# Optimization experiments

Hardware: AMD Instinct MI355X
Metric: run time of the kernel (lower is better)

Reference implementation:

```python
import jax, jax.numpy as jnp
import numpy as np

DIM = 512
NUM_ITEM = 2048
K = 10


def setup_inputs() -> dict:
    key = jax.random.key(0)
    k1, k2, k3 = jax.random.split(key, 3)
    input1 = jax.random.normal(k1, (16, DIM, 32, 32), dtype=jnp.float32)
    input2 = jax.random.normal(k2, (16, DIM, 32, 32), dtype=jnp.float32)
    stdv = 1.0 / np.sqrt(DIM)
    mempool = jax.random.uniform(k3, (NUM_ITEM, DIM), minval=-stdv, maxval=stdv, dtype=jnp.float32)
    return {"input1": input1, "input2": input2, "mempool": mempool}


def _memorize(x, mempool):
    # x: [B, C, H, W] with C == DIM
    B, C, H, W = x.shape
    q = jnp.transpose(x, (0, 2, 3, 1)).reshape(-1, C)      # [N, C]
    att = jax.nn.softmax(q @ mempool.T, axis=1)            # [N, num_item]
    val, idx = jax.lax.top_k(att, K)                       # [N, K]
    val = jax.nn.softmax(val, axis=1)                      # renormalize top-k
    # scatter(val into zeros) @ mempool == gather rows of mempool and combine
    out = jnp.einsum('nk,nkd->nd', val, mempool[idx])      # [N, C]
    return jnp.transpose(out.reshape(B, H, W, C), (0, 3, 1, 2))


def reference(input1, input2, mempool):
    return (_memorize(input1, mempool), _memorize(input2, mempool))
```

## Files before the change

kernel.cpp:

```cpp
#include <hip/hip_runtime.h>
#include <math.h>

typedef __attribute__((ext_vector_type(4))) float f4;
typedef __attribute__((ext_vector_type(8))) short bf16x8;
typedef __attribute__((ext_vector_type(4))) unsigned short u16x4;
typedef unsigned int u32;
typedef unsigned short u16;

#define DIMC  512
#define NITEM 2048
#define TK    10
#define WSP   (NITEM * DIMC)

#define TPB    512
#define PXB    64
#define RIT    256
#define NRND   8
#define NSLICE 16

#define MP_B   0
#define MP_PL  16384
#define SSTR   66
#define Q_B    67584
#define Q_PL   4096
#define LDS_BYTES 79872
#define MV_F 0
#define MI_F 5120
#define MM_F 10240
#define MS_F 10752
#define WB_F 11264
#define IB_F 11904

#define KSWZ(i) (((i) ^ ((i) >> 2)) & 3)

__device__ __forceinline__ u32 bf16_rne(float f) {
    u32 u = __float_as_uint(f);
    return (u + 0x7fffu + ((u >> 16) & 1u)) >> 16;
}

__global__ __launch_bounds__(256)
void preconv_kernel(const float* __restrict__ mp, u16* __restrict__ ws)
{
    int idx = (blockIdx.x * 256 + threadIdx.x) * 4;
    int i  = idx >> 9;
    int k0 = idx & 511;
    f4 v = *(const f4*)(mp + (size_t)i * 512 + k0);
    int s  = k0 >> 5, kl = k0 & 31;
    int pos = s * 32 + ((kl >> 2) & 3) * 8 + (kl >> 4) * 4;
    u16x4 p0, p1, p2;
#pragma unroll
    for (int e = 0; e < 4; ++e) {
        float f  = v[e];
        u32 b0   = bf16_rne(f);  float f0 = __uint_as_float(b0 << 16);
        float r1 = f - f0;
        u32 b1   = bf16_rne(r1); float f1 = __uint_as_float(b1 << 16);
        float r2 = r1 - f1;
        u32 b2   = bf16_rne(r2);
        p0[e] = (u16)b0; p1[e] = (u16)b1; p2[e] = (u16)b2;
    }
    size_t base = (size_t)i * 512 + pos;
    *(u16x4*)(ws + 0 * WSP + base) = p0;
    *(u16x4*)(ws + 1 * WSP + base) = p1;
    *(u16x4*)(ws + 2 * WSP + base) = p2;
}

__global__ __launch_bounds__(TPB, 4)
void memorize_mfma(const float* __restrict__ x0, const float* __restrict__ x1,
                   const float* __restrict__ mp, const u16* __restrict__ ws,
                   float* __restrict__ out)
{
    extern __shared__ char ldsb[];
    float* ldsf = (float*)ldsb;

    const int t    = threadIdx.x;
    const int lane = t & 63;
    const int w    = t >> 6;
    const int blk  = blockIdx.x;
    const int img  = blk >> 4;
    const int n0   = (blk & 15) * PXB;
    const int b    = img & 15;

    const float* x  = (img < 16) ? x0 : x1;
    const float* xb = x + (size_t)b * (DIMC * 1024);
    float* ob = out + (img < 16 ? (size_t)0 : (size_t)16 * DIMC * 1024)
                    + (size_t)b * (DIMC * 1024);

    const int l15 = lane & 15;
    const int lh  = lane >> 4;
    const int ksw = lh ^ KSWZ(l15);

    const int qp = t & 63;
    const int g  = t >> 6;

    float tv[TK]; int tix[TK];
#pragma unroll
    for (int q = 0; q < TK; ++q) { tv[q] = -INFINITY; tix[q] = 0x7fffffff; }
    float rm = -INFINITY, rs = 0.0f;

    const int scl  = t & 31;
    const int spx  = (t >> 5) << 2;
    const int spos = (((scl >> 2) & 3) << 3) + ((scl >> 4) << 2) + (scl & 3);
    const int sslot = spos >> 3;
    const int soff  = (spos & 7) << 1;

    const char* qb = ldsb + Q_B + (l15 << 6) + (ksw << 4);
    const char* ab = ldsb + MP_B + (size_t)((w << 5) + l15) * 64 + (ksw << 4);

    const int itq = lane >> 2;
    const int slo = lane & 3;
    const int ksrc = slo ^ KSWZ(itq);

#pragma unroll 1
    for (int r = 0; r < NRND; ++r) {
        f4 acc[2][4];
#pragma unroll
        for (int mt = 0; mt < 2; ++mt)
#pragma unroll
            for (int nt = 0; nt < 4; ++nt) acc[mt][nt] = (f4){0.f, 0.f, 0.f, 0.f};

#pragma unroll 1
        for (int s = 0; s < NSLICE; ++s) {
            __syncthreads();

            {
#pragma unroll
                for (int p = 0; p < 3; ++p) {
#pragma unroll
                    for (int qg = 0; qg < 2; ++qg) {
                        int I = (w << 5) + (qg << 4);
                        const u16* src = ws + (size_t)p * WSP
                                       + (size_t)(r * RIT + I + itq) * 512
                                       + (s << 5) + (ksrc << 3);
                        char* dst = ldsb + MP_B + p * MP_PL + I * 64;
                        __builtin_amdgcn_global_load_lds(
                            (const __attribute__((address_space(1))) u32*)src,
                            (__attribute__((address_space(3))) u32*)dst, 16, 0, 0);
                    }
                }
            }

            {
                const float* src = xb + (size_t)((s << 5) + scl) * 1024 + n0 + spx;
                f4 v = *(const f4*)src;
#pragma unroll
                for (int e = 0; e < 4; ++e) {
                    int px = spx + e;
                    float f  = v[e];
                    u32 b0   = bf16_rne(f);  float f0 = __uint_as_float(b0 << 16);
                    float r1 = f - f0;
                    u32 b1   = bf16_rne(r1); float f1 = __uint_as_float(b1 << 16);
                    float r2 = r1 - f1;
                    u32 b2   = bf16_rne(r2);
                    int ro = Q_B + (px << 6) + (((sslot ^ KSWZ(px)) << 4) | soff);
                    *(u16*)(ldsb + ro)            = (u16)b0;
                    *(u16*)(ldsb + ro + Q_PL)     = (u16)b1;
                    *(u16*)(ldsb + ro + 2 * Q_PL) = (u16)b2;
                }
            }
            __syncthreads();

            bf16x8 bq[4][3];
#pragma unroll
            for (int nt = 0; nt < 4; ++nt)
#pragma unroll
                for (int p = 0; p < 3; ++p)
                    bq[nt][p] = *(const bf16x8*)(qb + p * Q_PL + nt * 1024);

#pragma unroll
            for (int mt = 0; mt < 2; ++mt) {
                bf16x8 a0 = *(const bf16x8*)(ab + 0 * MP_PL + mt * 1024);
                bf16x8 a1 = *(const bf16x8*)(ab + 1 * MP_PL + mt * 1024);
                bf16x8 a2 = *(const bf16x8*)(ab + 2 * MP_PL + mt * 1024);
#pragma unroll
                for (int nt = 0; nt < 4; ++nt) {
                    f4 c = acc[mt][nt];
                    c = __builtin_amdgcn_mfma_f32_16x16x32_bf16(a0, bq[nt][0], c, 0, 0, 0);
                    c = __builtin_amdgcn_mfma_f32_16x16x32_bf16(a0, bq[nt][1], c, 0, 0, 0);
                    c = __builtin_amdgcn_mfma_f32_16x16x32_bf16(a1, bq[nt][0], c, 0, 0, 0);
                    c = __builtin_amdgcn_mfma_f32_16x16x32_bf16(a0, bq[nt][2], c, 0, 0, 0);
                    c = __builtin_amdgcn_mfma_f32_16x16x32_bf16(a1, bq[nt][1], c, 0, 0, 0);
                    c = __builtin_amdgcn_mfma_f32_16x16x32_bf16(a2, bq[nt][0], c, 0, 0, 0);
                    acc[mt][nt] = c;
                }
            }
        }

        __syncthreads();
#pragma unroll
        for (int mt = 0; mt < 2; ++mt) {
#pragma unroll
            for (int nt = 0; nt < 4; ++nt) {
                int row = (w << 5) + (mt << 4) + (lh << 2);
                int col = (nt << 4) + l15;
                float* sp = ldsf + row * SSTR + col;
                sp[0 * SSTR] = acc[mt][nt][0];
                sp[1 * SSTR] = acc[mt][nt][1];
                sp[2 * SSTR] = acc[mt][nt][2];
                sp[3 * SSTR] = acc[mt][nt][3];
            }
        }
        __syncthreads();

        float mloc = rm;
#pragma unroll 4
        for (int jj = 0; jj < 32; ++jj) {
            int   il = (g << 5) + jj;
            float v  = ldsf[il * SSTR + qp];
            mloc = fmaxf(mloc, v);
            if (v > tv[TK - 1]) {
                int   id = r * RIT + il;
                float cv = v; int ci = id;
#pragma unroll
                for (int q = 0; q < TK; ++q) {
                    bool  gt = cv > tv[q];
                    float nv = gt ? tv[q]  : cv;
                    int   ni = gt ? tix[q] : ci;
                    tv[q]  = gt ? cv : tv[q];
                    tix[q] = gt ? ci : tix[q];
                    cv = nv; ci = ni;
                }
            }
        }
        rs *= __expf(rm - mloc);
        rm = mloc;
#pragma unroll 4
        for (int jj = 0; jj < 32; ++jj) {
            int   il = (g << 5) + jj;
            float v  = ldsf[il * SSTR + qp];
            rs += __expf(v - rm);
        }
    }

    __syncthreads();
    {
#pragma unroll
        for (int q = 0; q < TK; ++q) {
            ldsf[MV_F + (qp * 8 + g) * TK + q] = tv[q];
            ldsf[MI_F + (qp * 8 + g) * TK + q] = __int_as_float(tix[q]);
        }
        ldsf[MM_F + qp * 8 + g] = rm;
        ldsf[MS_F + qp * 8 + g] = rs;
    }
    __syncthreads();

    if (t < 64) {
        const int p = t;
        float gm[8], gs[8];
#pragma unroll
        for (int G = 0; G < 8; ++G) {
            gm[G] = ldsf[MM_F + p * 8 + G];
            gs[G] = ldsf[MS_F + p * 8 + G];
        }
        float mstar = gm[0];
#pragma unroll
        for (int G = 1; G < 8; ++G) mstar = fmaxf(mstar, gm[G]);
        float Z = 0.0f;
#pragma unroll
        for (int G = 0; G < 8; ++G) Z += gs[G] * __expf(gm[G] - mstar);

        int h0=0,h1=0,h2=0,h3=0,h4=0,h5=0,h6=0,h7=0;
        float ov[TK]; int oi[TK];
#pragma unroll
        for (int o = 0; o < TK; ++o) {
            float bv = -INFINITY; int bi = 0x7fffffff; int bg = 0;
#define SEL(G, HG)                                                               \
            {                                                                    \
                float v  = ldsf[MV_F + (p * 8 + G) * TK + (HG)];                 \
                int   id = __float_as_int(ldsf[MI_F + (p * 8 + G) * TK + (HG)]); \
                if (v > bv || (v == bv && id < bi)) { bv = v; bi = id; bg = G; } \
            }
            SEL(0, h0) SEL(1, h1) SEL(2, h2) SEL(3, h3)
            SEL(4, h4) SEL(5, h5) SEL(6, h6) SEL(7, h7)
#undef SEL
            ov[o] = bv; oi[o] = bi;
            h0 += (bg == 0); h1 += (bg == 1); h2 += (bg == 2); h3 += (bg == 3);
            h4 += (bg == 4); h5 += (bg == 5); h6 += (bg == 6); h7 += (bg == 7);
        }
        float pv[TK];
#pragma unroll
        for (int o = 0; o < TK; ++o) pv[o] = __expf(ov[o] - mstar) / Z;
        float pmax = pv[0];
        float wgt[TK]; float W = 0.0f;
#pragma unroll
        for (int o = 0; o < TK; ++o) { wgt[o] = __expf(pv[o] - pmax); W += wgt[o]; }
#pragma unroll
        for (int o = 0; o < TK; ++o) {
            ldsf[WB_F + p * TK + o] = wgt[o] / W;
            ldsf[IB_F + p * TK + o] = __int_as_float(oi[o]);
        }
    }
    __syncthreads();

    {
        const int ep = t & 63, cg = t >> 6;
        float wr[TK]; const float* rows[TK];
#pragma unroll
        for (int o = 0; o < TK; ++o) {
            wr[o]   = ldsf[WB_F + ep * TK + o];
            rows[o] = mp + (size_t)__float_as_int(ldsf[IB_F + ep * TK + o]) * DIMC;
        }
        float* obase = ob + n0 + ep;
#pragma unroll 4
        for (int cc = 0; cc < 16; ++cc) {
            int c = cg * 64 + cc * 4;
            f4 a = {0.0f, 0.0f, 0.0f, 0.0f};
#pragma unroll
            for (int o = 0; o < TK; ++o) {
                f4 rv = *(const f4*)(rows[o] + c);
#pragma unroll
                for (int z = 0; z < 4; ++z) a[z] = fmaf(wr[o], rv[z], a[z]);
            }
#pragma unroll
            for (int z = 0; z < 4; ++z) obase[(size_t)(c + z) * 1024] = a[z];
        }
    }
}

extern "C" void kernel_launch(void* const* d_in, const int* in_sizes, int n_in,
                              void* d_out, int out_size, void* d_ws, size_t ws_size,
                              hipStream_t stream) {
    const float* x0  = (const float*)d_in[0];
    const float* x1  = (const float*)d_in[1];
    const float* mpl = (const float*)d_in[2];
    float* out = (float*)d_out;
    u16* ws = (u16*)d_ws;

    preconv_kernel<<<dim3(1024), dim3(256), 0, stream>>>(mpl, ws);
    memorize_mfma<<<dim3(512), dim3(TPB), LDS_BYTES, stream>>>(x0, x1, mpl, ws, out);
}
```

Before: 642.5 us.

## Switch to two-term fp16 split GEMM with double-buffered LDS staging

Replaces the three-way bf16 split (six MFMAs per tile) with a two-way fp16 split: a head plus a residual scaled by 2048, accumulated separately and recombined with a 1/2048 factor, so each tile needs three MFMAs. It also double-buffers the memory-pool and query tiles in LDS, so the next slice loads while the current one computes and one barrier per slice is removed. Accuracy is lower than the three-term bf16 split and could flip near-tied top-k picks. fp16 range limits are unlikely to matter for these inputs, and LDS use grows a little.

```diff
diff --git a/kernel.cpp b/kernel.cpp
--- a/kernel.cpp
+++ b/kernel.cpp
@@ -2,7 +2,7 @@
 #include <math.h>
 
 typedef __attribute__((ext_vector_type(4))) float f4;
-typedef __attribute__((ext_vector_type(8))) short bf16x8;
+typedef __attribute__((ext_vector_type(8))) _Float16 f16x8;
 typedef __attribute__((ext_vector_type(4))) unsigned short u16x4;
 typedef unsigned int u32;
 typedef unsigned short u16;
@@ -17,13 +17,15 @@
 #define RIT    256
 #define NRND   8
 #define NSLICE 16
-
-#define MP_B   0
+#define SCL    4.8828125e-4f
+
+#define MP_BUF 32768
 #define MP_PL  16384
+#define Q_BASE 65536
+#define Q_BUF  8192
+#define Q_PL   4096
 #define SSTR   66
-#define Q_B    67584
-#define Q_PL   4096
-#define LDS_BYTES 79872
+#define LDS_BYTES 81920
 #define MV_F 0
 #define MI_F 5120
 #define MM_F 10240
@@ -33,9 +35,13 @@
 
 #define KSWZ(i) (((i) ^ ((i) >> 2)) & 3)
 
-__device__ __forceinline__ u32 bf16_rne(float f) {
-    u32 u = __float_as_uint(f);
-    return (u + 0x7fffu + ((u >> 16) & 1u)) >> 16;
+union h16 { _Float16 h; u16 u; };
+
+__device__ __forceinline__ void split2(float f, u16& lo, u16& hi) {
+    h16 a; a.h = (_Float16)f;
+    float f0 = (float)a.h;
+    h16 b; b.h = (_Float16)((f - f0) * 2048.0f);
+    lo = a.u; hi = b.u;
 }
 
 __global__ __launch_bounds__(256)
@@ -47,21 +53,15 @@
     f4 v = *(const f4*)(mp + (size_t)i * 512 + k0);
     int s  = k0 >> 5, kl = k0 & 31;
     int pos = s * 32 + ((kl >> 2) & 3) * 8 + (kl >> 4) * 4;
-    u16x4 p0, p1, p2;
+    u16x4 p0, p1;
 #pragma unroll
     for (int e = 0; e < 4; ++e) {
-        float f  = v[e];
-        u32 b0   = bf16_rne(f);  float f0 = __uint_as_float(b0 << 16);
-        float r1 = f - f0;
-        u32 b1   = bf16_rne(r1); float f1 = __uint_as_float(b1 << 16);
-        float r2 = r1 - f1;
-        u32 b2   = bf16_rne(r2);
-        p0[e] = (u16)b0; p1[e] = (u16)b1; p2[e] = (u16)b2;
+        u16 lo, hi; split2(v[e], lo, hi);
+        p0[e] = lo; p1[e] = hi;
     }
     size_t base = (size_t)i * 512 + pos;
     *(u16x4*)(ws + 0 * WSP + base) = p0;
     *(u16x4*)(ws + 1 * WSP + base) = p1;
-    *(u16x4*)(ws + 2 * WSP + base) = p2;
 }
 
 __global__ __launch_bounds__(TPB, 4)
@@ -103,89 +103,94 @@
     const int sslot = spos >> 3;
     const int soff  = (spos & 7) << 1;
 
-    const char* qb = ldsb + Q_B + (l15 << 6) + (ksw << 4);
-    const char* ab = ldsb + MP_B + (size_t)((w << 5) + l15) * 64 + (ksw << 4);
-
     const int itq = lane >> 2;
     const int slo = lane & 3;
     const int ksrc = slo ^ KSWZ(itq);
 
+#define STAGE_MP(R, S, BUF)                                                    \
+    {                                                                          \
+        _Pragma("unroll")                                                      \
+        for (int p = 0; p < 2; ++p) {                                          \
+            _Pragma("unroll")                                                  \
+            for (int qg = 0; qg < 2; ++qg) {                                   \
+                int I = (w << 5) + (qg << 4);                                  \
+                const u16* src = ws + (size_t)p * WSP                          \
+                               + (size_t)((R) * RIT + I + itq) * 512           \
+                               + ((S) << 5) + (ksrc << 3);                     \
+                char* dst = ldsb + (BUF) * MP_BUF + p * MP_PL + I * 64;        \
+                __builtin_amdgcn_global_load_lds(                              \
+                    (const __attribute__((address_space(1))) u32*)src,         \
+                    (__attribute__((address_space(3))) u32*)dst, 16, 0, 0);    \
+            }                                                                  \
+        }                                                                      \
+    }
+
+#define STAGE_Q(S, BUF)                                                        \
+    {                                                                          \
+        const float* src = xb + (size_t)(((S) << 5) + scl) * 1024 + n0 + spx;  \
+        f4 v = *(const f4*)src;                                                \
+        _Pragma("unroll")                                                      \
+        for (int e = 0; e < 4; ++e) {                                          \
+            int px = spx + e;                                                  \
+            u16 lo, hi; split2(v[e], lo, hi);                                  \
+            int ro = Q_BASE + (BUF) * Q_BUF + (px << 6)                        \
+                   + (((sslot ^ KSWZ(px)) << 4) | soff);                       \
+            *(u16*)(ldsb + ro)        = lo;                                    \
+            *(u16*)(ldsb + ro + Q_PL) = hi;                                    \
+        }                                                                      \
+    }
+
 #pragma unroll 1
     for (int r = 0; r < NRND; ++r) {
-        f4 acc[2][4];
+        f4 acc0[2][4], acc1[2][4];
 #pragma unroll
         for (int mt = 0; mt < 2; ++mt)
 #pragma unroll
-            for (int nt = 0; nt < 4; ++nt) acc[mt][nt] = (f4){0.f, 0.f, 0.f, 0.f};
-
-#pragma unroll 1
+            for (int nt = 0; nt < 4; ++nt) {
+                acc0[mt][nt] = (f4){0.f, 0.f, 0.f, 0.f};
+                acc1[mt][nt] = (f4){0.f, 0.f, 0.f, 0.f};
+            }
+
+        __syncthreads();
+        STAGE_MP(r, 0, 0)
+        STAGE_Q(0, 0)
+        __syncthreads();
+
+#pragma unroll 2
         for (int s = 0; s < NSLICE; ++s) {
+            const int cur = s & 1;
+            if (s < NSLICE - 1) {
+                STAGE_MP(r, s + 1, cur ^ 1)
+                STAGE_Q(s + 1, cur ^ 1)
+            }
+
+            const char* qbc = ldsb + Q_BASE + cur * Q_BUF + (l15 << 6) + (ksw << 4);
+            const char* abc = ldsb + cur * MP_BUF + (size_t)((w << 5) + l15) * 64 + (ksw << 4);
+
+            f16x8 bq[4][2];
+#pragma unroll
+            for (int nt = 0; nt < 4; ++nt)
+#pragma unroll
+                for (int p = 0; p < 2; ++p)
+                    bq[nt][p] = *(const f16x8*)(qbc + p * Q_PL + nt * 1024);
+
+#pragma unroll
+            for (int mt = 0; mt < 2; ++mt) {
+                f16x8 a0 = *(const f16x8*)(abc + 0 * MP_PL + mt * 1024);
+                f16x8 a1 = *(const f16x8*)(abc + 1 * MP_PL + mt * 1024);
+#pragma unroll
+                for (int nt = 0; nt < 4; ++nt) {
+                    acc0[mt][nt] = __builtin_amdgcn_mfma_f32_16x16x32_f16(
+                        a0, bq[nt][0], acc0[mt][nt], 0, 0, 0);
+                    acc1[mt][nt] = __builtin_amdgcn_mfma_f32_16x16x32_f16(
+                        a0, bq[nt][1], acc1[mt][nt], 0, 0, 0);
+                    acc1[mt][nt] = __builtin_amdgcn_mfma_f32_16x16x32_f16(
+                        a1, bq[nt][0], acc1[mt][nt], 0, 0, 0);
+                }
+            }
             __syncthreads();
-
-            {
-#pragma unroll
-                for (int p = 0; p < 3; ++p) {
-#pragma unroll
-                    for (int qg = 0; qg < 2; ++qg) {
-                        int I = (w << 5) + (qg << 4);
-                        const u16* src = ws + (size_t)p * WSP
-                                       + (size_t)(r * RIT + I + itq) * 512
-                                       + (s << 5) + (ksrc << 3);
-                        char* dst = ldsb + MP_B + p * MP_PL + I * 64;
-                        __builtin_amdgcn_global_load_lds(
-                            (const __attribute__((address_space(1))) u32*)src,
-                            (__attribute__((address_space(3))) u32*)dst, 16, 0, 0);
-                    }
-                }
-            }
-
-            {
-                const float* src = xb + (size_t)((s << 5) + scl) * 1024 + n0 + spx;
-                f4 v = *(const f4*)src;
-#pragma unroll
-                for (int e = 0; e < 4; ++e) {
-                    int px = spx + e;
-                    float f  = v[e];
-                    u32 b0   = bf16_rne(f);  float f0 = __uint_as_float(b0 << 16);
-                    float r1 = f - f0;
-                    u32 b1   = bf16_rne(r1); float f1 = __uint_as_float(b1 << 16);
-                    float r2 = r1 - f1;
-                    u32 b2   = bf16_rne(r2);
-                    int ro = Q_B + (px << 6) + (((sslot ^ KSWZ(px)) << 4) | soff);
-                    *(u16*)(ldsb + ro)            = (u16)b0;
-                    *(u16*)(ldsb + ro + Q_PL)     = (u16)b1;
-                    *(u16*)(ldsb + ro + 2 * Q_PL) = (u16)b2;
-                }
-            }
-            __syncthreads();
-
-            bf16x8 bq[4][3];
-#pragma unroll
-            for (int nt = 0; nt < 4; ++nt)
-#pragma unroll
-                for (int p = 0; p < 3; ++p)
-                    bq[nt][p] = *(const bf16x8*)(qb + p * Q_PL + nt * 1024);
-
-#pragma unroll
-            for (int mt = 0; mt < 2; ++mt) {
-                bf16x8 a0 = *(const bf16x8*)(ab + 0 * MP_PL + mt * 1024);
-                bf16x8 a1 = *(const bf16x8*)(ab + 1 * MP_PL + mt * 1024);
-                bf16x8 a2 = *(const bf16x8*)(ab + 2 * MP_PL + mt * 1024);
-#pragma unroll
-                for (int nt = 0; nt < 4; ++nt) {
-                    f4 c = acc[mt][nt];
-                    c = __builtin_amdgcn_mfma_f32_16x16x32_bf16(a0, bq[nt][0], c, 0, 0, 0);
-                    c = __builtin_amdgcn_mfma_f32_16x16x32_bf16(a0, bq[nt][1], c, 0, 0, 0);
-                    c = __builtin_amdgcn_mfma_f32_16x16x32_bf16(a1, bq[nt][0], c, 0, 0, 0);
-                    c = __builtin_amdgcn_mfma_f32_16x16x32_bf16(a0, bq[nt][2], c, 0, 0, 0);
-                    c = __builtin_amdgcn_mfma_f32_16x16x32_bf16(a1, bq[nt][1], c, 0, 0, 0);
-                    c = __builtin_amdgcn_mfma_f32_16x16x32_bf16(a2, bq[nt][0], c, 0, 0, 0);
-                    acc[mt][nt] = c;
-                }
-            }
-        }
-
-        __syncthreads();
+        }
+
 #pragma unroll
         for (int mt = 0; mt < 2; ++mt) {
 #pragma unroll
@@ -193,10 +198,10 @@
                 int row = (w << 5) + (mt << 4) + (lh << 2);
                 int col = (nt << 4) + l15;
                 float* sp = ldsf + row * SSTR + col;
-                sp[0 * SSTR] = acc[mt][nt][0];
-                sp[1 * SSTR] = acc[mt][nt][1];
-                sp[2 * SSTR] = acc[mt][nt][2];
-                sp[3 * SSTR] = acc[mt][nt][3];
+                sp[0 * SSTR] = acc0[mt][nt][0] + SCL * acc1[mt][nt][0];
+                sp[1 * SSTR] = acc0[mt][nt][1] + SCL * acc1[mt][nt][1];
+                sp[2 * SSTR] = acc0[mt][nt][2] + SCL * acc1[mt][nt][2];
+                sp[3 * SSTR] = acc0[mt][nt][3] + SCL * acc1[mt][nt][3];
             }
         }
         __syncthreads();
@@ -314,6 +319,8 @@
             for (int z = 0; z < 4; ++z) obase[(size_t)(c + z) * 1024] = a[z];
         }
     }
+#undef STAGE_MP
+#undef STAGE_Q
 }
 
 extern "C" void kernel_launch(void* const* d_in, const int* in_sizes, int n_in,
```

New measurement: 939.0 us. 46.1% more time.
